# Optimization experiments

Measured on AMD Instinct MI355X. Metric: run time of the kernel, lower is better.

Reference implementation:

```python
import jax, jax.numpy as jnp
import numpy as np

WS = 7       # window size
NH = 2       # num heads
L = 256      # level_num == adaptive pool target
EPS_BN = 1e-5
EPS_LN = 1e-6

def _rel_idx():
    coords = np.stack(np.meshgrid(np.arange(WS), np.arange(WS), indexing='ij')).reshape(2, -1)
    rel = (coords[:, :, None] - coords[:, None, :]).transpose(1, 2, 0) + (WS - 1)
    return jnp.asarray(rel[..., 0] * (2 * WS - 1) + rel[..., 1])  # (49,49) int

REL_IDX = _rel_idx()

def _ln(x, g, b):
    m = x.mean(-1, keepdims=True)
    v = ((x - m) ** 2).mean(-1, keepdims=True)
    return (x - m) / jnp.sqrt(v + EPS_LN) * g + b

def _attn(t, H, W, qkv_w, qkv_b, proj_w, proj_b, rpe_table):
    # interlaced-pool (window) multi-head attention with relative position bias
    B, N, C = t.shape
    dh = C // NH
    ph, pw = (-H) % WS, (-W) % WS
    t4 = jnp.pad(t.reshape(B, H, W, C), ((0, 0), (0, ph), (0, pw), (0, 0)))
    Hp, Wp = H + ph, W + pw
    win = t4.reshape(B, Hp // WS, WS, Wp // WS, WS, C).transpose(0, 1, 3, 2, 4, 5).reshape(-1, WS * WS, C)
    M = win.shape[0]
    qkv = win @ qkv_w.T + qkv_b                       # (M,49,3C)
    q, k, v = jnp.split(qkv, 3, axis=-1)
    q = q.reshape(M, WS * WS, NH, dh)
    k = k.reshape(M, WS * WS, NH, dh)
    v = v.reshape(M, WS * WS, NH, dh)
    bias = rpe_table[REL_IDX].transpose(2, 0, 1)      # (NH,49,49)
    att = jnp.einsum('mqhd,mkhd->mhqk', q, k) / jnp.sqrt(jnp.float32(dh)) + bias
    att = jax.nn.softmax(att, axis=-1)
    o = jnp.einsum('mhqk,mkhd->mqhd', att, v).reshape(M, WS * WS, C)
    o = o @ proj_w.T + proj_b
    o = o.reshape(B, Hp // WS, Wp // WS, WS, WS, C).transpose(0, 1, 3, 2, 4, 5).reshape(B, Hp, Wp, C)
    return o[:, :H, :W, :].reshape(B, N, C)

def setup_inputs() -> dict:
    key = jax.random.key(0)
    ks = jax.random.split(key, 10)
    rn = lambda k, s, sc: (jax.random.normal(k, s, dtype=jnp.float32) * sc)
    return {
        'x': jax.random.normal(ks[0], (16, 256, 96, 96), dtype=jnp.float32),
        'conv1_w': rn(ks[1], (128, 256, 3, 3), 0.02),
        'bn1_g': jnp.ones((128,), jnp.float32), 'bn1_b': jnp.zeros((128,), jnp.float32),
        'bn1_m': jnp.zeros((128,), jnp.float32), 'bn1_v': jnp.ones((128,), jnp.float32),
        'ln_g': jnp.ones((128,), jnp.float32), 'ln_b': jnp.zeros((128,), jnp.float32),
        'qkv_w': rn(ks[2], (384, 128), 0.02), 'qkv_b': jnp.zeros((384,), jnp.float32),
        'proj_w': rn(ks[3], (128, 128), 0.02), 'proj_b': jnp.zeros((128,), jnp.float32),
        'rpe_table': rn(ks[4], (169, 2), 0.02),
        'conv2_w': rn(ks[5], (1, 128), 0.05),
        'f1_w': rn(ks[6], (64, 2), 0.2),
        'f2_w': rn(ks[7], (128, 64), 0.05),
        'out_w': rn(ks[8], (256, 128), 0.05),
        'obn_g': jnp.ones((256,), jnp.float32), 'obn_b': jnp.zeros((256,), jnp.float32),
        'obn_m': jnp.zeros((256,), jnp.float32), 'obn_v': jnp.ones((256,), jnp.float32),
        'gate': jnp.array(1.0, jnp.float32),
    }

def reference(x, conv1_w, bn1_g, bn1_b, bn1_m, bn1_v, ln_g, ln_b, qkv_w, qkv_b,
              proj_w, proj_b, rpe_table, conv2_w, f1_w, f2_w, out_w,
              obn_g, obn_b, obn_m, obn_v, gate):
    # conv1: 3x3 conv + BN + LeakyReLU
    x1 = jax.lax.conv_general_dilated(x, conv1_w, (1, 1), ((1, 1), (1, 1)),
                                      dimension_numbers=('NCHW', 'OIHW', 'NCHW'))
    x1 = (x1 - bn1_m[None, :, None, None]) / jnp.sqrt(bn1_v[None, :, None, None] + EPS_BN) \
         * bn1_g[None, :, None, None] + bn1_b[None, :, None, None]
    x1 = jnp.where(x1 > 0, x1, 0.01 * x1)
    B, C, H, W = x1.shape
    N = H * W
    tokens = x1.reshape(B, C, N).transpose(0, 2, 1)            # (B,N,128)
    s = _attn(_ln(tokens, ln_g, ln_b), H, W, qkv_w, qkv_b, proj_w, proj_b, rpe_table)
    s = s.transpose(0, 2, 1)                                   # (B,128,N)
    s = s.reshape(B, C, L, N // L).mean(-1)                    # AdaptiveAvgPool1d(256), exact (N % L == 0)
    s = s.mean(axis=1, keepdims=True)                          # (B,1,256)
    # conv2 -> sigmoid -> cos_sim
    cs = jax.nn.sigmoid(jnp.einsum('oi,bihw->bohw', conv2_w, x1)).reshape(B, N)
    # pandas-style unbiased (Fisher) kurtosis per sample
    n = jnp.float32(N)
    mu = cs.mean(-1, keepdims=True)
    d = cs - mu
    m2 = (d * d).sum(-1)
    m4 = (d ** 4).sum(-1)
    var = m2 / (n - 1)
    kurt = n * (n + 1) / ((n - 1) * (n - 2) * (n - 3)) * m4 / (var * var) \
           - 3 * (n - 1) ** 2 / ((n - 2) * (n - 3))
    K = jax.lax.stop_gradient(kurt)[:, None, None]             # detached in original (numpy roundtrip)
    cmin = cs.min(-1, keepdims=True)
    cmax = cs.max(-1, keepdims=True)
    ql = (2 * jnp.arange(L, dtype=jnp.float32) + 1) / (2 * L) * (cmax - cmin) + cmin  # (B,L)
    inter = (ql[:, 1] - ql[:, 0])[:, None, None]               # (B,1,1)
    quant = 1 - jnp.abs(ql[:, None, :] - cs[:, :, None])       # (B,N,L)
    quant = jnp.abs(K) * jnp.exp(-quant)                       # abs(K)/exp(quant)
    quant = jnp.where(quant > 1 - inter, quant, 0.0)
    sta = quant.sum(1)[:, None, :]                             # (B,1,L)
    sta = jnp.concatenate([gate * s, sta], axis=1)             # (B,2,L)
    h = jnp.einsum('oc,bcl->bol', f1_w, sta)
    h = jnp.where(h > 0, h, 0.01 * h)                          # f1 LeakyReLU
    h = jax.nn.relu(jnp.einsum('oc,bcl->bol', f2_w, h))        # f2 ReLU
    h = jnp.einsum('oc,bcl->bol', out_w, h)                    # out conv
    h = (h - obn_m[None, :, None]) / jnp.sqrt(obn_v[None, :, None] + EPS_BN) \
        * obn_g[None, :, None] + obn_b[None, :, None]
    h = jax.nn.relu(h)                                         # (B,256,256)
    return h, quant
```

## Files before the change

### kernel.cpp

```cpp
#include <hip/hip_runtime.h>
#include <math.h>

typedef unsigned short u16;
typedef short bf16x8 __attribute__((ext_vector_type(8)));
typedef float f32x4 __attribute__((ext_vector_type(4)));
typedef unsigned int uint4v __attribute__((ext_vector_type(4)));

#define NN   9216
#define CCH  128
#define LL   256

#define OFF_X1   0
#define OFF_CS   18874368
#define OFF_SPRE 19021824
#define OFF_STAQ 19025920
#define OFF_BSUM 19030016
#define OFF_BM2  19030032
#define OFF_BM4  19030048
#define OFF_BMAX 19030064
#define OFF_BMIN 19030080
#define OFF_PAR  19030096
#define OFF_WV   19030160
#define OFF_BV   19030416
#define OFF_PBS  19030418

#define PSTR 104

__device__ __forceinline__ unsigned rne16(float f) {
    unsigned u = __float_as_uint(f);
    return (u + 0x7FFFu + ((u >> 16) & 1u)) >> 16;
}

__global__ void k0_prep(const float* __restrict__ qkv_w, const float* __restrict__ qkv_b,
                        const float* __restrict__ proj_w, const float* __restrict__ proj_b,
                        float* __restrict__ wsf) {
    __shared__ float psum[128];
    int t = threadIdx.x;
    if (t < 128) {
        float s = 0.f;
        for (int c = 0; c < 128; ++c) s += proj_w[c * 128 + t];
        psum[t] = s;
    }
    __syncthreads();
    {
        int h = t >> 7, c = t & 127;
        float s = 0.f;
        for (int j = 0; j < 64; ++j)
            s += qkv_w[(size_t)(256 + h * 64 + j) * 128 + c] * psum[h * 64 + j];
        wsf[OFF_WV + h * 128 + c] = s;
    }
    if (t < 2) {
        float s = 0.f;
        for (int j = 0; j < 64; ++j) s += qkv_b[256 + t * 64 + j] * psum[t * 64 + j];
        wsf[OFF_BV + t] = s;
    }
    if (t == 0) {
        float s = 0.f;
        for (int c = 0; c < 128; ++c) s += proj_b[c];
        wsf[OFF_PBS] = s;
    }
}

__global__ __launch_bounds__(256) void k0c_wsplit(
    const float* __restrict__ w, const float* __restrict__ g, const float* __restrict__ bb,
    const float* __restrict__ m, const float* __restrict__ v,
    u16* __restrict__ bsh, u16* __restrict__ bsm, u16* __restrict__ bsl,
    float* __restrict__ bo) {
    int idx = blockIdx.x * 256 + threadIdx.x;
    int j    = idx & 7;
    int lane = (idx >> 3) & 63;
    int nfg  = (idx >> 9) & 7;
    int icb  = (idx >> 12) & 7;
    int t    = idx >> 15;
    int oc = nfg * 16 + (lane & 15);
    int ic = icb * 32 + ((lane >> 4) << 3) + j;
    float sc = g[oc] / sqrtf(v[oc] + 1e-5f);
    float wv = w[(size_t)(oc * 256 + ic) * 9 + t] * sc;
    unsigned hb = rne16(wv);
    float hf = __uint_as_float(hb << 16);
    float r1 = wv - hf;
    unsigned mb = rne16(r1);
    float mfv = __uint_as_float(mb << 16);
    float r2 = r1 - mfv;
    unsigned lb = rne16(r2);
    bsh[idx] = (u16)hb;
    bsm[idx] = (u16)mb;
    bsl[idx] = (u16)lb;
    if (blockIdx.x == 0 && threadIdx.x < 128) {
        int o = threadIdx.x;
        float s2 = g[o] / sqrtf(v[o] + 1e-5f);
        bo[o] = bb[o] - m[o] * s2;
    }
}

__global__ __launch_bounds__(256) void k1_mfma(
    const float* __restrict__ x,
    const u16* __restrict__ bsh, const u16* __restrict__ bsm, const u16* __restrict__ bsl,
    const float* __restrict__ bo,
    float* __restrict__ x1) {
    __shared__ __align__(16) u16 P[10 * 18 * PSTR];
    int tid = threadIdx.x;
    int lane = tid & 63, wave = tid >> 6;
    int wm = wave >> 1, wn = wave & 1;
    int l15 = lane & 15, lg = lane >> 4;
    int tile = blockIdx.x, ocg = blockIdx.y, b = blockIdx.z;
    int y0 = (tile / 6) * 8, x0 = (tile % 6) * 16;
    const float* xb = x + (size_t)b * 256 * NN;

    int srow = tid / 18, scol = tid - srow * 18;
    int gy = y0 - 1 + srow, gx = x0 - 1 + scol;
    bool sval = (tid < 180) && gy >= 0 && gy < 96 && gx >= 0 && gx < 96;
    const float* pbase = xb + (size_t)(gy >= 0 ? (gy < 96 ? gy : 95) : 0) * 96
                            + (gx >= 0 ? (gx < 96 ? gx : 95) : 0);
    int pb = tid * PSTR;

    f32x4 acc[4][2];
#pragma unroll
    for (int mf = 0; mf < 4; ++mf)
#pragma unroll
        for (int nf = 0; nf < 2; ++nf) acc[mf][nf] = (f32x4){0.f, 0.f, 0.f, 0.f};

    int nfg0 = ocg * 4 + wn * 2;

    for (int icb = 0; icb < 8; ++icb) {
        __syncthreads();
        if (tid < 180) {
            const float* pic = pbase + (size_t)icb * 32 * NN;
#pragma unroll
            for (int g = 0; g < 4; ++g) {
                unsigned hw[4], mw[4], lw[4];
#pragma unroll
                for (int jj = 0; jj < 4; ++jj) {
                    float v0 = sval ? pic[(size_t)(g * 8 + 2 * jj) * NN] : 0.f;
                    float v1 = sval ? pic[(size_t)(g * 8 + 2 * jj + 1) * NN] : 0.f;
                    unsigned h0 = rne16(v0); float hf0 = __uint_as_float(h0 << 16);
                    float r0 = v0 - hf0;     unsigned m0 = rne16(r0);
                    float mf0 = __uint_as_float(m0 << 16);
                    unsigned l0 = rne16(r0 - mf0);
                    unsigned h1 = rne16(v1); float hf1 = __uint_as_float(h1 << 16);
                    float r1 = v1 - hf1;     unsigned m1 = rne16(r1);
                    float mf1 = __uint_as_float(m1 << 16);
                    unsigned l1 = rne16(r1 - mf1);
                    hw[jj] = h0 | (h1 << 16);
                    mw[jj] = m0 | (m1 << 16);
                    lw[jj] = l0 | (l1 << 16);
                }
                *(uint4v*)&P[pb + (g * 3 + 0) * 8] = (uint4v){hw[0], hw[1], hw[2], hw[3]};
                *(uint4v*)&P[pb + (g * 3 + 1) * 8] = (uint4v){mw[0], mw[1], mw[2], mw[3]};
                *(uint4v*)&P[pb + (g * 3 + 2) * 8] = (uint4v){lw[0], lw[1], lw[2], lw[3]};
            }
        }
        __syncthreads();
#pragma unroll
        for (int t = 0; t < 9; ++t) {
            const int dy = t / 3, dx = t - dy * 3;
            bf16x8 Bh[2], Bm[2], Bl[2];
#pragma unroll
            for (int nf = 0; nf < 2; ++nf) {
                size_t boff = ((((size_t)t * 8 + icb) * 8 + (nfg0 + nf)) * 64 + lane) * 8;
                Bh[nf] = *(const bf16x8*)(bsh + boff);
                Bm[nf] = *(const bf16x8*)(bsm + boff);
                Bl[nf] = *(const bf16x8*)(bsl + boff);
            }
#pragma unroll
            for (int mf = 0; mf < 4; ++mf) {
                int abase = ((wm * 4 + mf + dy) * 18 + dx + l15) * PSTR + lg * 24;
                bf16x8 Ah = *(const bf16x8*)&P[abase];
                bf16x8 Am = *(const bf16x8*)&P[abase + 8];
                bf16x8 Al = *(const bf16x8*)&P[abase + 16];
#pragma unroll
                for (int nf = 0; nf < 2; ++nf) {
                    f32x4 a = acc[mf][nf];
                    a = __builtin_amdgcn_mfma_f32_16x16x32_bf16(Ah, Bh[nf], a, 0, 0, 0);
                    a = __builtin_amdgcn_mfma_f32_16x16x32_bf16(Am, Bh[nf], a, 0, 0, 0);
                    a = __builtin_amdgcn_mfma_f32_16x16x32_bf16(Ah, Bm[nf], a, 0, 0, 0);
                    a = __builtin_amdgcn_mfma_f32_16x16x32_bf16(Al, Bh[nf], a, 0, 0, 0);
                    a = __builtin_amdgcn_mfma_f32_16x16x32_bf16(Ah, Bl[nf], a, 0, 0, 0);
                    a = __builtin_amdgcn_mfma_f32_16x16x32_bf16(Am, Bm[nf], a, 0, 0, 0);
                    acc[mf][nf] = a;
                }
            }
        }
    }
#pragma unroll
    for (int nf = 0; nf < 2; ++nf) {
        int oc = ocg * 64 + wn * 32 + nf * 16 + l15;
        float bov = bo[oc];
#pragma unroll
        for (int mf = 0; mf < 4; ++mf) {
            int py = y0 + wm * 4 + mf;
            int px = x0 + lg * 4;
            float4 r;
            float t0;
            t0 = acc[mf][nf].x + bov; r.x = t0 > 0.f ? t0 : 0.01f * t0;
            t0 = acc[mf][nf].y + bov; r.y = t0 > 0.f ? t0 : 0.01f * t0;
            t0 = acc[mf][nf].z + bov; r.z = t0 > 0.f ? t0 : 0.01f * t0;
            t0 = acc[mf][nf].w + bov; r.w = t0 > 0.f ? t0 : 0.01f * t0;
            *(float4*)&x1[((size_t)b * 128 + oc) * NN + py * 96 + px] = r;
        }
    }
}

__global__ __launch_bounds__(256) void k3_attn(
    const float* __restrict__ x1, const float* __restrict__ ln_g, const float* __restrict__ ln_b,
    const float* __restrict__ qkv_w, const float* __restrict__ qkv_b,
    const float* __restrict__ rpe, const float* __restrict__ wsf,
    float* __restrict__ spre) {
    __shared__ __align__(16) float T[49 * 132];
    __shared__ __align__(16) float Qs[49 * 132];
    __shared__ __align__(16) float Ks[49 * 132];
    __shared__ float vps[49 * 2];
    __shared__ float mstat[49], rstat[49];
    int tid = threadIdx.x;
    int wwin = blockIdx.x, b = blockIdx.y;
    int wh = wwin / 14, ww = wwin % 14;

    for (int idx = tid; idx < 128 * 49; idx += 256) {
        int c = idx / 49, i = idx % 49;
        int th = wh * 7 + i / 7, tw = ww * 7 + i % 7;
        float vv = 0.f;
        if (th < 96 && tw < 96) vv = x1[((size_t)b * 128 + c) * NN + th * 96 + tw];
        T[i * 132 + c] = vv;
    }
    __syncthreads();
    if (tid < 49) {
        float s = 0.f;
        for (int c4 = 0; c4 < 128; c4 += 4) {
            float4 t4 = *(const float4*)&T[tid * 132 + c4];
            s += t4.x + t4.y + t4.z + t4.w;
        }
        float mean = s * (1.f / 128.f);
        float vs = 0.f;
        for (int c4 = 0; c4 < 128; c4 += 4) {
            float4 t4 = *(const float4*)&T[tid * 132 + c4];
            float d0 = t4.x - mean, d1 = t4.y - mean, d2 = t4.z - mean, d3 = t4.w - mean;
            vs += d0 * d0 + d1 * d1 + d2 * d2 + d3 * d3;
        }
        mstat[tid] = mean;
        rstat[tid] = 1.f / sqrtf(vs * (1.f / 128.f) + 1e-6f);
    }
    __syncthreads();
    for (int idx = tid; idx < 49 * 128; idx += 256) {
        int i = idx >> 7, c = idx & 127;
        int th = wh * 7 + i / 7, tw = ww * 7 + i % 7;
        float vv = T[i * 132 + c];
        float nv = (vv - mstat[i]) * rstat[i] * ln_g[c] + ln_b[c];
        T[i * 132 + c] = (th < 96 && tw < 96) ? nv : 0.f;
    }
    __syncthreads();
    {
        int o2 = (tid & 127) * 2;
        int i0 = (tid >> 7) * 24;
        float a0[25], a1[25];
#pragma unroll
        for (int ii = 0; ii < 25; ++ii) { a0[ii] = 0.f; a1[ii] = 0.f; }
        for (int cc = 0; cc < 128; cc += 4) {
            float4 wa = *(const float4*)&qkv_w[(size_t)o2 * 128 + cc];
            float4 wc = *(const float4*)&qkv_w[(size_t)(o2 + 1) * 128 + cc];
#pragma unroll
            for (int ii = 0; ii < 25; ++ii) {
                float4 t4 = *(const float4*)&T[(i0 + ii) * 132 + cc];
                a0[ii] += t4.x * wa.x + t4.y * wa.y + t4.z * wa.z + t4.w * wa.w;
                a1[ii] += t4.x * wc.x + t4.y * wc.y + t4.z * wc.z + t4.w * wc.w;
            }
        }
        float bq0 = qkv_b[o2], bq1 = qkv_b[o2 + 1];
        float* dst = (o2 < 128) ? Qs : Ks;
        int oo = o2 & 127;
#pragma unroll
        for (int ii = 0; ii < 25; ++ii) {
            dst[(i0 + ii) * 132 + oo]     = a0[ii] + bq0;
            dst[(i0 + ii) * 132 + oo + 1] = a1[ii] + bq1;
        }
    }
    if (tid < 98) {
        int i = tid >> 1, h = tid & 1;
        float s = wsf[OFF_BV + h];
        for (int c = 0; c < 128; ++c) s += T[i * 132 + c] * wsf[OFF_WV + h * 128 + c];
        vps[i * 2 + h] = s;
    }
    __syncthreads();
    {
        int h = tid >> 7, i = tid & 127;
        if (i < 49) {
            float qr[64];
#pragma unroll
            for (int d4 = 0; d4 < 64; d4 += 4) {
                float4 q4 = *(const float4*)&Qs[i * 132 + h * 64 + d4];
                qr[d4] = q4.x; qr[d4 + 1] = q4.y; qr[d4 + 2] = q4.z; qr[d4 + 3] = q4.w;
            }
            int ih7 = i / 7, iw7 = i % 7;
            for (int j = 0; j < 49; ++j) {
                float s = 0.f;
#pragma unroll
                for (int d4 = 0; d4 < 64; d4 += 4) {
                    float4 k4 = *(const float4*)&Ks[j * 132 + h * 64 + d4];
                    s += qr[d4] * k4.x + qr[d4 + 1] * k4.y + qr[d4 + 2] * k4.z + qr[d4 + 3] * k4.w;
                }
                int relidx = (ih7 - j / 7 + 6) * 13 + (iw7 - j % 7 + 6);
                T[(h * 49 + i) * 52 + j] = s * 0.125f + rpe[relidx * 2 + h];
            }
        }
    }
    __syncthreads();
    {
        int h = tid >> 7, i = tid & 127;
        if (i < 49) {
            float r[49];
            float* row = &T[(h * 49 + i) * 52];
#pragma unroll
            for (int j = 0; j < 49; ++j) r[j] = row[j];
            float mx = r[0];
#pragma unroll
            for (int j = 1; j < 49; ++j) mx = fmaxf(mx, r[j]);
            float sum = 0.f;
#pragma unroll
            for (int j = 0; j < 49; ++j) { r[j] = expf(r[j] - mx); sum += r[j]; }
            float inv = 1.f / sum;
#pragma unroll
            for (int j = 0; j < 49; ++j) row[j] = r[j] * inv;
        }
    }
    __syncthreads();
    if (tid < 49) {
        int i = tid;
        int th = wh * 7 + i / 7, tw = ww * 7 + i % 7;
        float s = wsf[OFF_PBS];
        for (int h = 0; h < 2; ++h)
            for (int j = 0; j < 49; ++j)
                s += T[(h * 49 + i) * 52 + j] * vps[j * 2 + h];
        if (th < 96 && tw < 96) {
            int l = (th * 96 + tw) / 36;
            atomicAdd(&spre[b * 256 + l], s);
        }
    }
}

__global__ __launch_bounds__(256) void k4_cs(
    const float* __restrict__ x1, const float* __restrict__ w2,
    float* __restrict__ csb, float* __restrict__ bsum,
    unsigned* __restrict__ bmin, unsigned* __restrict__ bmax) {
    int b = blockIdx.y;
    int n = blockIdx.x * 256 + threadIdx.x;
    float s = 0.f;
    for (int c = 0; c < 128; ++c) s += w2[c] * x1[((size_t)b * 128 + c) * NN + n];
    float csv = 1.f / (1.f + expf(-s));
    csb[(size_t)b * NN + n] = csv;
    float ss = csv, mn = csv, mx = csv;
    for (int o = 32; o > 0; o >>= 1) {
        ss += __shfl_down(ss, o, 64);
        mn = fminf(mn, __shfl_down(mn, o, 64));
        mx = fmaxf(mx, __shfl_down(mx, o, 64));
    }
    if ((threadIdx.x & 63) == 0) {
        atomicAdd(&bsum[b], ss);
        atomicMin(&bmin[b], __float_as_uint(mn));
        atomicMax(&bmax[b], __float_as_uint(mx));
    }
}

__global__ __launch_bounds__(256) void k5_mom(
    const float* __restrict__ csb, const float* __restrict__ bsum,
    float* __restrict__ bm2, float* __restrict__ bm4) {
    int b = blockIdx.y;
    int n = blockIdx.x * 256 + threadIdx.x;
    float mu = bsum[b] * (1.f / 9216.f);
    float d = csb[(size_t)b * NN + n] - mu;
    float d2 = d * d, d4 = d2 * d2;
    for (int o = 32; o > 0; o >>= 1) {
        d2 += __shfl_down(d2, o, 64);
        d4 += __shfl_down(d4, o, 64);
    }
    if ((threadIdx.x & 63) == 0) { atomicAdd(&bm2[b], d2); atomicAdd(&bm4[b], d4); }
}

__global__ void k5b_par(const float* __restrict__ bsum, const float* __restrict__ bm2,
                        const float* __restrict__ bm4, const unsigned* __restrict__ bmin,
                        const unsigned* __restrict__ bmax, float* __restrict__ par) {
    int b = threadIdx.x;
    if (b >= 16) return;
    float n = 9216.f;
    float m2 = bm2[b], m4 = bm4[b];
    float var = m2 / (n - 1.f);
    float t1 = n * (n + 1.f) / ((n - 1.f) * (n - 2.f) * (n - 3.f)) * m4 / (var * var);
    float t2 = 3.f * ((n - 1.f) * (n - 1.f)) / ((n - 2.f) * (n - 3.f));
    float kurt = t1 - t2;
    float cmin = __uint_as_float(bmin[b]);
    float cmax = __uint_as_float(bmax[b]);
    float range = cmax - cmin;
    float ql0 = (1.f / 512.f) * range + cmin;
    float ql1 = (3.f / 512.f) * range + cmin;
    float inter = ql1 - ql0;
    par[b * 4 + 0] = fabsf(kurt);
    par[b * 4 + 1] = cmin;
    par[b * 4 + 2] = range;
    par[b * 4 + 3] = 1.f - inter;
}

__global__ __launch_bounds__(256) void k6_quant(
    const float* __restrict__ csb, const float* __restrict__ par,
    float* __restrict__ outq, float* __restrict__ staq) {
    int b = blockIdx.y;
    int n0 = blockIdx.x * 64;
    int l = threadIdx.x;
    float absK = par[b * 4 + 0], cmin = par[b * 4 + 1];
    float range = par[b * 4 + 2], thr = par[b * 4 + 3];
    float qlv = ((float)(2 * l + 1) * (1.f / 512.f)) * range + cmin;
    float lsum = 0.f;
    for (int j = 0; j < 64; ++j) {
        float csv = csb[(size_t)b * NN + n0 + j];
        float d = fabsf(qlv - csv);
        float q0 = 1.f - d;
        float qv = absK * expf(-q0);
        float o = (qv > thr) ? qv : 0.f;
        outq[((size_t)(b * NN + n0 + j)) * 256 + l] = o;
        lsum += o;
    }
    atomicAdd(&staq[b * 256 + l], lsum);
}

__global__ __launch_bounds__(256) void k7_head(
    const float* __restrict__ spre, const float* __restrict__ staq,
    const float* __restrict__ f1w, const float* __restrict__ f2w,
    const float* __restrict__ ow, const float* __restrict__ og,
    const float* __restrict__ ob, const float* __restrict__ om,
    const float* __restrict__ ov, const float* __restrict__ gate,
    float* __restrict__ out0) {
    __shared__ float in0[16], in1[16];
    __shared__ float h1[16][64];
    __shared__ __align__(16) float h2[16][132];
    int tid = threadIdx.x;
    int lt = blockIdx.x, b = blockIdx.y;
    if (tid < 16) {
        int l = lt * 16 + tid;
        in0[tid] = gate[0] * (spre[b * 256 + l] * (1.f / 4608.f));
        in1[tid] = staq[b * 256 + l];
    }
    __syncthreads();
    for (int idx = tid; idx < 16 * 64; idx += 256) {
        int j = idx >> 6, o = idx & 63;
        float vv = f1w[o * 2] * in0[j] + f1w[o * 2 + 1] * in1[j];
        h1[j][o] = vv > 0.f ? vv : 0.01f * vv;
    }
    __syncthreads();
    for (int idx = tid; idx < 16 * 128; idx += 256) {
        int j = idx >> 7, o = idx & 127;
        float s = 0.f;
        for (int c = 0; c < 64; ++c) s += f2w[o * 64 + c] * h1[j][c];
        h2[j][o] = fmaxf(s, 0.f);
    }
    __syncthreads();
    {
        int o = tid;
        float acc[16];
#pragma unroll
        for (int j = 0; j < 16; ++j) acc[j] = 0.f;
        for (int c4 = 0; c4 < 128; c4 += 4) {
            float4 w4 = *(const float4*)&ow[(size_t)o * 128 + c4];
#pragma unroll
            for (int j = 0; j < 16; ++j) {
                float4 hh = *(const float4*)&h2[j][c4];
                acc[j] += w4.x * hh.x + w4.y * hh.y + w4.z * hh.z + w4.w * hh.w;
            }
        }
        float sc = og[o] / sqrtf(ov[o] + 1e-5f);
        float bo = ob[o] - om[o] * sc;
        float res[16];
#pragma unroll
        for (int j = 0; j < 16; ++j) { float vv = acc[j] * sc + bo; res[j] = fmaxf(vv, 0.f); }
        float* dst = &out0[((size_t)b * 256 + o) * 256 + lt * 16];
#pragma unroll
        for (int q = 0; q < 4; ++q)
            ((float4*)dst)[q] = make_float4(res[q * 4], res[q * 4 + 1], res[q * 4 + 2], res[q * 4 + 3]);
    }
}

extern "C" void kernel_launch(void* const* d_in, const int* in_sizes, int n_in,
                              void* d_out, int out_size, void* d_ws, size_t ws_size,
                              hipStream_t stream) {
    const float* x       = (const float*)d_in[0];
    const float* conv1_w = (const float*)d_in[1];
    const float* bn1_g   = (const float*)d_in[2];
    const float* bn1_b   = (const float*)d_in[3];
    const float* bn1_m   = (const float*)d_in[4];
    const float* bn1_v   = (const float*)d_in[5];
    const float* ln_g    = (const float*)d_in[6];
    const float* ln_b    = (const float*)d_in[7];
    const float* qkv_w   = (const float*)d_in[8];
    const float* qkv_b   = (const float*)d_in[9];
    const float* proj_w  = (const float*)d_in[10];
    const float* proj_b  = (const float*)d_in[11];
    const float* rpe     = (const float*)d_in[12];
    const float* conv2_w = (const float*)d_in[13];
    const float* f1_w    = (const float*)d_in[14];
    const float* f2_w    = (const float*)d_in[15];
    const float* out_w   = (const float*)d_in[16];
    const float* obn_g   = (const float*)d_in[17];
    const float* obn_b   = (const float*)d_in[18];
    const float* obn_m   = (const float*)d_in[19];
    const float* obn_v   = (const float*)d_in[20];
    const float* gate    = (const float*)d_in[21];
    float* wsf  = (float*)d_ws;
    float* out0 = (float*)d_out;
    float* outq = out0 + 1048576;

    u16* bsh = (u16*)outq;
    u16* bsm = bsh + 294912;
    u16* bsl = bsm + 294912;
    float* bo = (float*)(bsl + 294912);

    hipMemsetAsync(wsf + OFF_SPRE, 0, (size_t)(OFF_BMIN - OFF_SPRE) * 4, stream);
    hipMemsetAsync(wsf + OFF_BMIN, 0xFF, 16 * 4, stream);

    hipLaunchKernelGGL(k0_prep, dim3(1), dim3(256), 0, stream, qkv_w, qkv_b, proj_w, proj_b, wsf);
    hipLaunchKernelGGL(k0c_wsplit, dim3(1152), dim3(256), 0, stream,
                       conv1_w, bn1_g, bn1_b, bn1_m, bn1_v, bsh, bsm, bsl, bo);
    hipLaunchKernelGGL(k1_mfma, dim3(72, 2, 16), dim3(256), 0, stream,
                       x, bsh, bsm, bsl, bo, wsf + OFF_X1);
    hipLaunchKernelGGL(k4_cs, dim3(36, 16), dim3(256), 0, stream,
                       wsf + OFF_X1, conv2_w, wsf + OFF_CS, wsf + OFF_BSUM,
                       (unsigned*)(wsf + OFF_BMIN), (unsigned*)(wsf + OFF_BMAX));
    hipLaunchKernelGGL(k5_mom, dim3(36, 16), dim3(256), 0, stream,
                       wsf + OFF_CS, wsf + OFF_BSUM, wsf + OFF_BM2, wsf + OFF_BM4);
    hipLaunchKernelGGL(k5b_par, dim3(1), dim3(64), 0, stream,
                       wsf + OFF_BSUM, wsf + OFF_BM2, wsf + OFF_BM4,
                       (const unsigned*)(wsf + OFF_BMIN), (const unsigned*)(wsf + OFF_BMAX),
                       wsf + OFF_PAR);
    hipLaunchKernelGGL(k3_attn, dim3(196, 16), dim3(256), 0, stream,
                       wsf + OFF_X1, ln_g, ln_b, qkv_w, qkv_b, rpe, wsf, wsf + OFF_SPRE);
    hipLaunchKernelGGL(k6_quant, dim3(144, 16), dim3(256), 0, stream,
                       wsf + OFF_CS, wsf + OFF_PAR, outq, wsf + OFF_STAQ);
    hipLaunchKernelGGL(k7_head, dim3(16, 16), dim3(256), 0, stream,
                       wsf + OFF_SPRE, wsf + OFF_STAQ, f1_w, f2_w, out_w,
                       obn_g, obn_b, obn_m, obn_v, gate, out0);
}
```

Baseline: 1.278 ms.

## Move window attention QK projection and scores onto bf16 MFMA

Rewrites the window-attention kernel so the Q/K projection and the QK^T score computation run as bf16 MFMA matmuls instead of scalar fp32 FMAs. The prep kernel now also pre-packs qkv_w into bf16 in MFMA fragment order. The LayerNorm statistics are parallelised across 4 lanes per token with shuffles, and the rpe table is staged in shared memory. This trades fp32 precision for bf16 in Q, K and the normalised activations, which may change results slightly.

```diff
diff --git a/kernel.cpp b/kernel.cpp
--- a/kernel.cpp
+++ b/kernel.cpp
@@ -23,6 +23,7 @@
 #define OFF_WV   19030160
 #define OFF_BV   19030416
 #define OFF_PBS  19030418
+#define OFF_WQK  19030432
 
 #define PSTR 104
 
@@ -58,6 +59,16 @@
         float s = 0.f;
         for (int c = 0; c < 128; ++c) s += proj_b[c];
         wsf[OFF_PBS] = s;
+    }
+    u16* wqk = (u16*)(wsf + OFF_WQK);
+    for (int idx = t; idx < 32768; idx += 256) {
+        int j = idx & 7;
+        int lane = (idx >> 3) & 63;
+        int ng = (idx >> 9) & 15;
+        int ks = idx >> 13;
+        int och = ng * 16 + (lane & 15);
+        int c = ks * 32 + ((lane >> 4) << 3) + j;
+        wqk[idx] = (u16)rne16(qkv_w[(size_t)och * 128 + c]);
     }
 }
 
@@ -203,132 +214,179 @@
 
 __global__ __launch_bounds__(256) void k3_attn(
     const float* __restrict__ x1, const float* __restrict__ ln_g, const float* __restrict__ ln_b,
-    const float* __restrict__ qkv_w, const float* __restrict__ qkv_b,
-    const float* __restrict__ rpe, const float* __restrict__ wsf,
-    float* __restrict__ spre) {
-    __shared__ __align__(16) float T[49 * 132];
-    __shared__ __align__(16) float Qs[49 * 132];
-    __shared__ __align__(16) float Ks[49 * 132];
+    const float* __restrict__ qkv_b, const float* __restrict__ rpe,
+    const float* __restrict__ wsf, float* __restrict__ spre) {
+    __shared__ __align__(16) float SM[49 * 132];
+    __shared__ __align__(16) u16 Ts[64 * 136];
+    __shared__ __align__(16) u16 Qs[64 * 136];
+    __shared__ __align__(16) u16 Ks[64 * 136];
     __shared__ float vps[49 * 2];
     __shared__ float mstat[49], rstat[49];
+    __shared__ float rpe_s[338];
     int tid = threadIdx.x;
+    int lane = tid & 63, wave = tid >> 6;
+    int l15 = lane & 15, lg = lane >> 4;
     int wwin = blockIdx.x, b = blockIdx.y;
     int wh = wwin / 14, ww = wwin % 14;
+    const u16* wqk = (const u16*)(wsf + OFF_WQK);
 
     for (int idx = tid; idx < 128 * 49; idx += 256) {
-        int c = idx / 49, i = idx % 49;
-        int th = wh * 7 + i / 7, tw = ww * 7 + i % 7;
+        int c = idx / 49, i = idx - c * 49;
+        int th = wh * 7 + (i * 37 >> 8), tw = ww * 7 + (i - (i * 37 >> 8) * 7);
         float vv = 0.f;
         if (th < 96 && tw < 96) vv = x1[((size_t)b * 128 + c) * NN + th * 96 + tw];
-        T[i * 132 + c] = vv;
-    }
-    __syncthreads();
-    if (tid < 49) {
+        SM[i * 132 + c] = vv;
+    }
+    if (tid < 338) rpe_s[tid] = rpe[tid];
+    __syncthreads();
+    if (tid < 196) {
+        int i = tid >> 2, p = tid & 3;
         float s = 0.f;
-        for (int c4 = 0; c4 < 128; c4 += 4) {
-            float4 t4 = *(const float4*)&T[tid * 132 + c4];
+        for (int c4 = 0; c4 < 32; c4 += 4) {
+            float4 t4 = *(const float4*)&SM[i * 132 + p * 32 + c4];
             s += t4.x + t4.y + t4.z + t4.w;
         }
+        s += __shfl_xor(s, 1, 64);
+        s += __shfl_xor(s, 2, 64);
         float mean = s * (1.f / 128.f);
         float vs = 0.f;
-        for (int c4 = 0; c4 < 128; c4 += 4) {
-            float4 t4 = *(const float4*)&T[tid * 132 + c4];
+        for (int c4 = 0; c4 < 32; c4 += 4) {
+            float4 t4 = *(const float4*)&SM[i * 132 + p * 32 + c4];
             float d0 = t4.x - mean, d1 = t4.y - mean, d2 = t4.z - mean, d3 = t4.w - mean;
             vs += d0 * d0 + d1 * d1 + d2 * d2 + d3 * d3;
         }
-        mstat[tid] = mean;
-        rstat[tid] = 1.f / sqrtf(vs * (1.f / 128.f) + 1e-6f);
-    }
-    __syncthreads();
-    for (int idx = tid; idx < 49 * 128; idx += 256) {
+        vs += __shfl_xor(vs, 1, 64);
+        vs += __shfl_xor(vs, 2, 64);
+        if (p == 0) {
+            mstat[i] = mean;
+            rstat[i] = 1.f / sqrtf(vs * (1.f / 128.f) + 1e-6f);
+        }
+    }
+    __syncthreads();
+    for (int idx = tid; idx < 64 * 128; idx += 256) {
         int i = idx >> 7, c = idx & 127;
-        int th = wh * 7 + i / 7, tw = ww * 7 + i % 7;
-        float vv = T[i * 132 + c];
-        float nv = (vv - mstat[i]) * rstat[i] * ln_g[c] + ln_b[c];
-        T[i * 132 + c] = (th < 96 && tw < 96) ? nv : 0.f;
+        u16 out = 0;
+        if (i < 49) {
+            int i7 = i * 37 >> 8;
+            int th = wh * 7 + i7, tw = ww * 7 + (i - i7 * 7);
+            if (th < 96 && tw < 96) {
+                float nv = (SM[i * 132 + c] - mstat[i]) * rstat[i] * ln_g[c] + ln_b[c];
+                out = (u16)rne16(nv);
+            }
+        }
+        Ts[i * 136 + c] = out;
     }
     __syncthreads();
     {
-        int o2 = (tid & 127) * 2;
-        int i0 = (tid >> 7) * 24;
-        float a0[25], a1[25];
-#pragma unroll
-        for (int ii = 0; ii < 25; ++ii) { a0[ii] = 0.f; a1[ii] = 0.f; }
-        for (int cc = 0; cc < 128; cc += 4) {
-            float4 wa = *(const float4*)&qkv_w[(size_t)o2 * 128 + cc];
-            float4 wc = *(const float4*)&qkv_w[(size_t)(o2 + 1) * 128 + cc];
-#pragma unroll
-            for (int ii = 0; ii < 25; ++ii) {
-                float4 t4 = *(const float4*)&T[(i0 + ii) * 132 + cc];
-                a0[ii] += t4.x * wa.x + t4.y * wa.y + t4.z * wa.z + t4.w * wa.w;
-                a1[ii] += t4.x * wc.x + t4.y * wc.y + t4.z * wc.z + t4.w * wc.w;
-            }
-        }
-        float bq0 = qkv_b[o2], bq1 = qkv_b[o2 + 1];
-        float* dst = (o2 < 128) ? Qs : Ks;
-        int oo = o2 & 127;
-#pragma unroll
-        for (int ii = 0; ii < 25; ++ii) {
-            dst[(i0 + ii) * 132 + oo]     = a0[ii] + bq0;
-            dst[(i0 + ii) * 132 + oo + 1] = a1[ii] + bq1;
+        f32x4 qacc[4][4];
+#pragma unroll
+        for (int mf = 0; mf < 4; ++mf)
+#pragma unroll
+            for (int nf = 0; nf < 4; ++nf) qacc[mf][nf] = (f32x4){0.f, 0.f, 0.f, 0.f};
+        for (int ks = 0; ks < 4; ++ks) {
+            bf16x8 Bv[4];
+#pragma unroll
+            for (int nf = 0; nf < 4; ++nf)
+                Bv[nf] = *(const bf16x8*)&wqk[(((size_t)ks * 16 + wave * 4 + nf) * 64 + lane) * 8];
+#pragma unroll
+            for (int mf = 0; mf < 4; ++mf) {
+                bf16x8 Av = *(const bf16x8*)&Ts[(mf * 16 + l15) * 136 + ks * 32 + lg * 8];
+#pragma unroll
+                for (int nf = 0; nf < 4; ++nf)
+                    qacc[mf][nf] = __builtin_amdgcn_mfma_f32_16x16x32_bf16(Av, Bv[nf], qacc[mf][nf], 0, 0, 0);
+            }
+        }
+#pragma unroll
+        for (int nf = 0; nf < 4; ++nf) {
+            int och = wave * 64 + nf * 16 + l15;
+            float bias = qkv_b[och];
+            u16* dst = (och < 128) ? Qs : Ks;
+            int ch = och & 127;
+#pragma unroll
+            for (int mf = 0; mf < 4; ++mf) {
+#pragma unroll
+                for (int r = 0; r < 4; ++r) {
+                    int tok = mf * 16 + lg * 4 + r;
+                    dst[tok * 136 + ch] = (u16)rne16(qacc[mf][nf][r] + bias);
+                }
+            }
         }
     }
     if (tid < 98) {
         int i = tid >> 1, h = tid & 1;
         float s = wsf[OFF_BV + h];
-        for (int c = 0; c < 128; ++c) s += T[i * 132 + c] * wsf[OFF_WV + h * 128 + c];
+        for (int c = 0; c < 128; ++c)
+            s += __uint_as_float((unsigned)Ts[i * 136 + c] << 16) * wsf[OFF_WV + h * 128 + c];
         vps[i * 2 + h] = s;
     }
     __syncthreads();
     {
-        int h = tid >> 7, i = tid & 127;
-        if (i < 49) {
-            float qr[64];
-#pragma unroll
-            for (int d4 = 0; d4 < 64; d4 += 4) {
-                float4 q4 = *(const float4*)&Qs[i * 132 + h * 64 + d4];
-                qr[d4] = q4.x; qr[d4 + 1] = q4.y; qr[d4 + 2] = q4.z; qr[d4 + 3] = q4.w;
-            }
-            int ih7 = i / 7, iw7 = i % 7;
-            for (int j = 0; j < 49; ++j) {
-                float s = 0.f;
-#pragma unroll
-                for (int d4 = 0; d4 < 64; d4 += 4) {
-                    float4 k4 = *(const float4*)&Ks[j * 132 + h * 64 + d4];
-                    s += qr[d4] * k4.x + qr[d4 + 1] * k4.y + qr[d4 + 2] * k4.z + qr[d4 + 3] * k4.w;
+        int h = wave >> 1, jh = wave & 1;
+        f32x4 sacc[4][2];
+#pragma unroll
+        for (int mf = 0; mf < 4; ++mf)
+#pragma unroll
+            for (int nf = 0; nf < 2; ++nf) sacc[mf][nf] = (f32x4){0.f, 0.f, 0.f, 0.f};
+        for (int ks = 0; ks < 2; ++ks) {
+            bf16x8 Bv[2];
+#pragma unroll
+            for (int nf = 0; nf < 2; ++nf)
+                Bv[nf] = *(const bf16x8*)&Ks[(jh * 32 + nf * 16 + l15) * 136 + h * 64 + ks * 32 + lg * 8];
+#pragma unroll
+            for (int mf = 0; mf < 4; ++mf) {
+                bf16x8 Av = *(const bf16x8*)&Qs[(mf * 16 + l15) * 136 + h * 64 + ks * 32 + lg * 8];
+#pragma unroll
+                for (int nf = 0; nf < 2; ++nf)
+                    sacc[mf][nf] = __builtin_amdgcn_mfma_f32_16x16x32_bf16(Av, Bv[nf], sacc[mf][nf], 0, 0, 0);
+            }
+        }
+        __syncthreads();
+#pragma unroll
+        for (int nf = 0; nf < 2; ++nf) {
+            int j = jh * 32 + nf * 16 + l15;
+            if (j < 49) {
+                int j7 = j * 37 >> 8, jm = j - j7 * 7;
+#pragma unroll
+                for (int mf = 0; mf < 4; ++mf) {
+#pragma unroll
+                    for (int r = 0; r < 4; ++r) {
+                        int i = mf * 16 + lg * 4 + r;
+                        if (i < 49) {
+                            int i7 = i * 37 >> 8, im = i - i7 * 7;
+                            int rel = (i7 - j7 + 6) * 13 + (im - jm + 6);
+                            SM[(h * 49 + i) * 52 + j] = sacc[mf][nf][r] * 0.125f + rpe_s[rel * 2 + h];
+                        }
+                    }
                 }
-                int relidx = (ih7 - j / 7 + 6) * 13 + (iw7 - j % 7 + 6);
-                T[(h * 49 + i) * 52 + j] = s * 0.125f + rpe[relidx * 2 + h];
-            }
-        }
-    }
-    __syncthreads();
-    {
-        int h = tid >> 7, i = tid & 127;
-        if (i < 49) {
-            float r[49];
-            float* row = &T[(h * 49 + i) * 52];
-#pragma unroll
-            for (int j = 0; j < 49; ++j) r[j] = row[j];
-            float mx = r[0];
-#pragma unroll
-            for (int j = 1; j < 49; ++j) mx = fmaxf(mx, r[j]);
-            float sum = 0.f;
-#pragma unroll
-            for (int j = 0; j < 49; ++j) { r[j] = expf(r[j] - mx); sum += r[j]; }
-            float inv = 1.f / sum;
-#pragma unroll
-            for (int j = 0; j < 49; ++j) row[j] = r[j] * inv;
-        }
+            }
+        }
+    }
+    __syncthreads();
+    if (tid < 98) {
+        int h = tid / 49, i = tid - h * 49;
+        float r[49];
+        float* row = &SM[(h * 49 + i) * 52];
+#pragma unroll
+        for (int j = 0; j < 49; ++j) r[j] = row[j];
+        float mx = r[0];
+#pragma unroll
+        for (int j = 1; j < 49; ++j) mx = fmaxf(mx, r[j]);
+        float sum = 0.f;
+#pragma unroll
+        for (int j = 0; j < 49; ++j) { r[j] = expf(r[j] - mx); sum += r[j]; }
+        float inv = 1.f / sum;
+#pragma unroll
+        for (int j = 0; j < 49; ++j) row[j] = r[j] * inv;
     }
     __syncthreads();
     if (tid < 49) {
         int i = tid;
-        int th = wh * 7 + i / 7, tw = ww * 7 + i % 7;
+        int i7 = i * 37 >> 8;
+        int th = wh * 7 + i7, tw = ww * 7 + (i - i7 * 7);
         float s = wsf[OFF_PBS];
         for (int h = 0; h < 2; ++h)
             for (int j = 0; j < 49; ++j)
-                s += T[(h * 49 + i) * 52 + j] * vps[j * 2 + h];
+                s += SM[(h * 49 + i) * 52 + j] * vps[j * 2 + h];
         if (th < 96 && tw < 96) {
             int l = (th * 96 + tw) / 36;
             atomicAdd(&spre[b * 256 + l], s);
@@ -527,7 +585,7 @@
                        (const unsigned*)(wsf + OFF_BMIN), (const unsigned*)(wsf + OFF_BMAX),
                        wsf + OFF_PAR);
     hipLaunchKernelGGL(k3_attn, dim3(196, 16), dim3(256), 0, stream,
-                       wsf + OFF_X1, ln_g, ln_b, qkv_w, qkv_b, rpe, wsf, wsf + OFF_SPRE);
+                       wsf + OFF_X1, ln_g, ln_b, qkv_b, rpe, wsf, wsf + OFF_SPRE);
     hipLaunchKernelGGL(k6_quant, dim3(144, 16), dim3(256), 0, stream,
                        wsf + OFF_CS, wsf + OFF_PAR, outq, wsf + OFF_STAQ);
     hipLaunchKernelGGL(k7_head, dim3(16, 16), dim3(256), 0, stream,
```

New measurement: 1.053 ms. -17.6%, faster.
